# Kernel optimization log

Measured on AMD Instinct MI355X. Metric: run time of the kernel, lower is better.

The kernel has to match this reference:

```python
import jax, jax.numpy as jnp
import numpy as np

WS = (8, 8)          # window size (Wh, Ww)
SS = (4, 4)          # shift size
DIM = 512
HEADS = 16
HD = DIM // HEADS    # 32
D1 = (HD // 2) // 2  # 8
D2 = (HD // 2) - D1  # 8
EPS = 1e-5
B, H, W = 4, 128, 128
HIDDEN = int(DIM * 4.0)  # 2048 (swiglu -> fc1 out = 2*HIDDEN)


def _layer_norm(x, g, b):
    m = jnp.mean(x, -1, keepdims=True)
    v = jnp.mean((x - m) ** 2, -1, keepdims=True)
    return (x - m) * jax.lax.rsqrt(v + EPS) * g + b


def _rope_tables():
    wh, ww = WS
    inv1 = 10000.0 ** (-(jnp.arange(D1, dtype=jnp.float32) / D1))
    inv2 = 10000.0 ** (-(jnp.arange(D2, dtype=jnp.float32) / D2))
    rows = jnp.arange(wh, dtype=jnp.float32)[:, None] * inv1  # (wh, D1)
    cols = jnp.arange(ww, dtype=jnp.float32)[:, None] * inv2  # (ww, D2)
    sin1 = jnp.broadcast_to(jnp.sin(rows)[:, None, :], (wh, ww, D1))
    cos1 = jnp.broadcast_to(jnp.cos(rows)[:, None, :], (wh, ww, D1))
    sin2 = jnp.broadcast_to(jnp.sin(cols)[None, :, :], (wh, ww, D2))
    cos2 = jnp.broadcast_to(jnp.cos(cols)[None, :, :], (wh, ww, D2))
    return sin1, cos1, sin2, cos2


def _rope2d(t, tabs):
    # t: (B_*heads, wh, ww, HD)
    sin1, cos1, sin2, cos2 = tabs
    x11 = t[..., :D1]
    x21 = t[..., D1:D1 + D2]
    x12 = t[..., D1 + D2:D1 + D2 + D1]
    x22 = t[..., D1 + D2 + D1:]
    return jnp.concatenate([
        x11 * cos1 - x12 * sin1,
        x21 * cos2 - x22 * sin2,
        x12 * cos1 + x11 * sin1,
        x22 * cos2 + x21 * sin2,
    ], axis=-1)


def _swin_mask():
    wh, ww = WS
    img = np.zeros((H, W), dtype=np.float32)
    cnt = 0
    for hs in (slice(0, -wh), slice(-wh, -SS[0]), slice(-SS[0], None)):
        for ws in (slice(0, -ww), slice(-ww, -SS[1]), slice(-SS[1], None)):
            img[hs, ws] = cnt
            cnt += 1
    mw = img.reshape(H // wh, wh, W // ww, ww).transpose(0, 2, 1, 3).reshape(-1, wh * ww)
    diff = mw[:, None, :] - mw[:, :, None]
    return jnp.asarray(np.where(diff != 0, -100.0, 0.0).astype(np.float32))


def setup_inputs() -> dict:
    key = jax.random.key(0)
    ks = jax.random.split(key, 14)
    s = 0.02
    return {
        "x": jax.random.normal(ks[0], (B, H, W, DIM), jnp.float32),
        "attn_mask": _swin_mask(),
        "norm1_g": jnp.ones((DIM,), jnp.float32),
        "norm1_b": jnp.zeros((DIM,), jnp.float32),
        "qkv_w": jax.random.normal(ks[1], (3 * DIM, DIM), jnp.float32) * s,
        "qkv_b": jnp.zeros((3 * DIM,), jnp.float32),
        "proj_w": jax.random.normal(ks[2], (DIM, DIM), jnp.float32) * s,
        "proj_b": jnp.zeros((DIM,), jnp.float32),
        "norm2_g": jnp.ones((DIM,), jnp.float32),
        "norm2_b": jnp.zeros((DIM,), jnp.float32),
        "fc1_w": jax.random.normal(ks[3], (2 * HIDDEN, DIM), jnp.float32) * s,
        "fc1_b": jnp.zeros((2 * HIDDEN,), jnp.float32),
        "fc2_w": jax.random.normal(ks[4], (DIM, HIDDEN), jnp.float32) * s,
        "fc2_b": jnp.zeros((DIM,), jnp.float32),
    }


def reference(x, attn_mask, norm1_g, norm1_b, qkv_w, qkv_b, proj_w, proj_b,
              norm2_g, norm2_b, fc1_w, fc1_b, fc2_w, fc2_b):
    wh, ww = WS
    N = wh * ww
    nH, nW = H // wh, W // ww
    nWin = nH * nW
    B_ = B * nWin
    tabs = _rope_tables()

    shortcut = x
    xn = _layer_norm(x, norm1_g, norm1_b)
    # cyclic shift
    xs = jnp.roll(xn, (-SS[0], -SS[1]), axis=(1, 2))
    # window partition: (B,H,W,C) -> (B*nWin, N, C)
    xw = xs.reshape(B, nH, wh, nW, ww, DIM).transpose(0, 1, 3, 2, 4, 5).reshape(B_, N, DIM)

    qkv = xw @ qkv_w.T + qkv_b
    qkv = qkv.reshape(B_, N, 3, HEADS, HD).transpose(2, 0, 3, 1, 4)  # (3,B_,h,N,hd)
    q, k, v = qkv[0], qkv[1], qkv[2]
    # inline 2D RoPE on q,k per window
    q = _rope2d(q.reshape(-1, wh, ww, HD), tabs).reshape(B_, HEADS, N, HD)
    k = _rope2d(k.reshape(-1, wh, ww, HD), tabs).reshape(B_, HEADS, N, HD)

    scale = HD ** -0.5
    attn = jnp.einsum('bhnd,bhmd->bhnm', q * scale, k)
    attn = attn.reshape(B, nWin, HEADS, N, N) + attn_mask[None, :, None]
    attn = jax.nn.softmax(attn.reshape(B_, HEADS, N, N), axis=-1)

    out = jnp.einsum('bhnm,bhmd->bhnd', attn, v).transpose(0, 2, 1, 3).reshape(B_, N, DIM)
    out = out @ proj_w.T + proj_b
    # window reverse + reverse shift
    out = out.reshape(B, nH, nW, wh, ww, DIM).transpose(0, 1, 3, 2, 4, 5).reshape(B, H, W, DIM)
    out = jnp.roll(out, (SS[0], SS[1]), axis=(1, 2))

    x = shortcut + out
    # SwiGLU MLP
    y = _layer_norm(x, norm2_g, norm2_b)
    h = y @ fc1_w.T + fc1_b
    a, gate = jnp.split(h, 2, axis=-1)
    h = jax.nn.silu(gate) * a
    y = h @ fc2_w.T + fc2_b
    return x + y
```

## Files before the change

kernel.cpp:

```cpp
#include <hip/hip_runtime.h>
#include <stdint.h>

typedef __attribute__((ext_vector_type(8))) short bf16x8;
typedef __attribute__((ext_vector_type(4))) float f32x4;
typedef __attribute__((ext_vector_type(4))) int i32x4;
typedef unsigned short u16;

#define GLD_LDS16(g, l) __builtin_amdgcn_global_load_lds( \
    (const __attribute__((address_space(1))) void*)(g),   \
    (__attribute__((address_space(3))) void*)(l), 16, 0, 0)

#define PB() do { __builtin_amdgcn_sched_barrier(0); \
                  __builtin_amdgcn_s_barrier();      \
                  __builtin_amdgcn_sched_barrier(0); } while (0)

#define ACCUM(d, a_, b_) d = __builtin_amdgcn_mfma_f32_16x16x32_bf16(a_, b_, d, 0, 0, 0)
#define ACCI(d, a_, b_)  d = __builtin_amdgcn_mfma_i32_16x16x64_i8(a_, b_, d, 0, 0, 0)

#define INV_A (1.0f / 16384.0f)
#define INV_P (1.0f / 32768.0f)
#define INV_H (1.0f / 65536.0f)

__device__ __forceinline__ u16 f2bf(float f) {
  union { float f; uint32_t u; } a; a.f = f;
  uint32_t u = a.u;
  return (u16)((u + 0x7fffu + ((u >> 16) & 1u)) >> 16);
}
__device__ __forceinline__ float bf2f(u16 h) {
  union { uint32_t u; float f; } a; a.u = ((uint32_t)h) << 16;
  return a.f;
}
__device__ __forceinline__ uint32_t q8x4(float a, float b, float c, float d, float s) {
  int qa = (int)rintf(fminf(fmaxf(a * s, -127.f), 127.f));
  int qb = (int)rintf(fminf(fmaxf(b * s, -127.f), 127.f));
  int qc = (int)rintf(fminf(fmaxf(c * s, -127.f), 127.f));
  int qd = (int)rintf(fminf(fmaxf(d * s, -127.f), 127.f));
  return (qa & 255) | ((qb & 255) << 8) | ((qc & 255) << 16) | ((qd & 255) << 24);
}
__device__ __forceinline__ char q8(float v, float s) {
  return (char)(int)rintf(fminf(fmaxf(v * s, -127.f), 127.f));
}

__global__ __launch_bounds__(256) void ln1_wconv(const float* __restrict__ x,
    const float* __restrict__ gw, const float* __restrict__ bw, char* __restrict__ out,
    const float* __restrict__ qw, const float* __restrict__ pw,
    const float* __restrict__ f1w, const float* __restrict__ f2w,
    char* __restrict__ wb8) {
  int bx = blockIdx.x;
  if (bx >= 16384) {
    int i4 = (bx - 16384) * 1024 + threadIdx.x * 4;
    float w[4];
#pragma unroll
    for (int j = 0; j < 4; j++) {
      int idx = i4 + j;
      if (idx < 786432)        w[j] = qw[idx];
      else if (idx < 1048576)  w[j] = pw[idx - 786432];
      else if (idx < 3145728)  w[j] = f1w[idx - 1048576];
      else                     w[j] = f2w[idx - 3145728];
    }
    *(uint32_t*)(wb8 + i4) = q8x4(w[0], w[1], w[2], w[3], 1024.f);
    return;
  }
  int wid = threadIdx.x >> 6;
  int lane = threadIdx.x & 63;
  int m = (bx << 2) + wid;
  int n = m & 63;
  int bwin = m >> 6;
  int b = bwin >> 8;
  int wi = bwin & 255;
  int h = (((wi >> 4) << 3) + (n >> 3) + 4) & 127;
  int w = (((wi & 15) << 3) + (n & 7) + 4) & 127;
  const float* src = x + (((size_t)((b << 7) + h) << 7) + (size_t)w) * 512;
  int ch = lane << 3;
  float4 v0 = *(const float4*)(src + ch);
  float4 v1 = *(const float4*)(src + ch + 4);
  float vv[8] = {v0.x, v0.y, v0.z, v0.w, v1.x, v1.y, v1.z, v1.w};
  float s = 0.f, s2 = 0.f;
#pragma unroll
  for (int j = 0; j < 8; j++) { s += vv[j]; s2 += vv[j] * vv[j]; }
#pragma unroll
  for (int off = 32; off; off >>= 1) {
    s += __shfl_xor(s, off);
    s2 += __shfl_xor(s2, off);
  }
  float mean = s * (1.f / 512.f);
  float var = s2 * (1.f / 512.f) - mean * mean;
  float rstd = rsqrtf(var + 1e-5f);
  float y[8];
#pragma unroll
  for (int j = 0; j < 8; j++) y[j] = (vv[j] - mean) * rstd * gw[ch + j] + bw[ch + j];
  uint2 o;
  o.x = q8x4(y[0], y[1], y[2], y[3], 16.f);
  o.y = q8x4(y[4], y[5], y[6], y[7], 16.f);
  *(uint2*)(out + ((size_t)m << 9) + ch) = o;
}

__global__ __launch_bounds__(256) void ln2_q8(const u16* __restrict__ sb,
    const float* __restrict__ gw, const float* __restrict__ bw,
    char* __restrict__ out) {
  int wid = threadIdx.x >> 6;
  int lane = threadIdx.x & 63;
  int m = (blockIdx.x << 2) + wid;
  int ch = lane << 3;
  union { uint4 u; u16 hh[8]; } in;
  in.u = *(const uint4*)(sb + ((size_t)m << 9) + ch);
  float vv[8];
#pragma unroll
  for (int j = 0; j < 8; j++) vv[j] = bf2f(in.hh[j]);
  float s = 0.f, s2 = 0.f;
#pragma unroll
  for (int j = 0; j < 8; j++) { s += vv[j]; s2 += vv[j] * vv[j]; }
#pragma unroll
  for (int off = 32; off; off >>= 1) {
    s += __shfl_xor(s, off);
    s2 += __shfl_xor(s2, off);
  }
  float mean = s * (1.f / 512.f);
  float var = s2 * (1.f / 512.f) - mean * mean;
  float rstd = rsqrtf(var + 1e-5f);
  float y[8];
#pragma unroll
  for (int j = 0; j < 8; j++) y[j] = (vv[j] - mean) * rstd * gw[ch + j] + bw[ch + j];
  uint2 o;
  o.x = q8x4(y[0], y[1], y[2], y[3], 16.f);
  o.y = q8x4(y[4], y[5], y[6], y[7], 16.f);
  *(uint2*)(out + ((size_t)m << 9) + ch) = o;
}

template<int EPI, int K>
__global__ __launch_bounds__(512, 1) void gemm8i(
    const char* __restrict__ A, const char* __restrict__ Bw,
    const float* __restrict__ bias, void* __restrict__ outp,
    const float* __restrict__ resid, int NTN) {
  __shared__ __align__(16) char lds[2][4][16384];
  const int NT = K / 128;
  int bid = blockIdx.x;
  int nwg = gridDim.x;
  int wg = (bid & 7) * (nwg >> 3) + (bid >> 3);
  int mt = wg / NTN, nt = wg - mt * NTN;
  int m0 = mt << 8;
  int n0 = (EPI == 3) ? (nt << 7) : (nt << 8);

  int tid = threadIdx.x;
  int wid = tid >> 6, lane = tid & 63;
  int wm = wid >> 2, wn = wid & 3;
  int l15 = lane & 15, lhi = lane >> 4;
  int swz = (lane & 7) << 4;

  int sr0 = tid >> 3;
  int xk = (((tid & 7) ^ ((tid >> 3) & 7)) << 4);

  auto stage = [&](int mat, int hh, int t) {
    if (t >= NT) return;
    char* ld = &lds[t & 1][mat * 2 + hh][0] + (wid << 10);
    const char* g0;
    if (mat == 0) {
      g0 = A + (size_t)(m0 + hh * 128 + sr0) * K + t * 128 + xk;
    } else {
      int rb;
      if (EPI == 3) rb = (hh ? 2048 : 0) + n0 + sr0;
      else          rb = n0 + hh * 128 + sr0;
      g0 = Bw + (size_t)rb * K + t * 128 + xk;
    }
    GLD_LDS16(g0, ld);
    GLD_LDS16(g0 + (size_t)64 * K, ld + 8192);
  };

  i32x4 acc[2][4][2][2] = {};
  i32x4 afr[4][2], b1r[2][2];
  i32x4 b0A[2][2], b0B[2][2];

  int aoffB = (wm * 64 + l15) * 128;
  int boffB = (wn * 32 + l15) * 128;
  int k0b = (lhi * 16) ^ swz;
  int k1b = (64 + lhi * 16) ^ swz;

  stage(0, 0, 0); stage(1, 1, 0); stage(1, 0, 0); stage(0, 1, 0);
  stage(0, 0, 1); stage(1, 1, 1);
  asm volatile("s_waitcnt vmcnt(4)" ::: "memory");
  __builtin_amdgcn_sched_barrier(0);
  __builtin_amdgcn_s_barrier();
  __builtin_amdgcn_sched_barrier(0);
  {
    const char* B00 = &lds[0][2][0];
#pragma unroll
    for (int j = 0; j < 2; j++) {
      b0A[j][0] = *(const i32x4*)&B00[boffB + j * 2048 + k0b];
      b0A[j][1] = *(const i32x4*)&B00[boffB + j * 2048 + k1b];
    }
  }

  auto tile = [&](int s, i32x4 (&b0c)[2][2], i32x4 (&b0n)[2][2]) {
    const char* Ah0 = &lds[s & 1][0][0];
    const char* Ah1 = &lds[s & 1][1][0];
    const char* Bh1 = &lds[s & 1][3][0];
    const char* Bn0 = &lds[(s + 1) & 1][2][0];

#pragma unroll
    for (int i = 0; i < 4; i++) {
      afr[i][0] = *(const i32x4*)&Ah0[aoffB + i * 2048 + k0b];
      afr[i][1] = *(const i32x4*)&Ah0[aoffB + i * 2048 + k1b];
    }
    stage(1, 0, s + 1);
    PB();
    __builtin_amdgcn_s_setprio(1);
#pragma unroll
    for (int i = 0; i < 4; i++)
#pragma unroll
      for (int j = 0; j < 2; j++) {
        ACCI(acc[0][i][0][j], afr[i][0], b0c[j][0]);
        ACCI(acc[0][i][0][j], afr[i][1], b0c[j][1]);
      }
    __builtin_amdgcn_s_setprio(0);
    PB();

#pragma unroll
    for (int j = 0; j < 2; j++) {
      b1r[j][0] = *(const i32x4*)&Bh1[boffB + j * 2048 + k0b];
      b1r[j][1] = *(const i32x4*)&Bh1[boffB + j * 2048 + k1b];
    }
    stage(0, 1, s + 1);
    PB();
    __builtin_amdgcn_s_setprio(1);
#pragma unroll
    for (int i = 0; i < 4; i++)
#pragma unroll
      for (int j = 0; j < 2; j++) {
        ACCI(acc[0][i][1][j], afr[i][0], b1r[j][0]);
        ACCI(acc[0][i][1][j], afr[i][1], b1r[j][1]);
      }
    __builtin_amdgcn_s_setprio(0);
    PB();

#pragma unroll
    for (int i = 0; i < 4; i++) {
      afr[i][0] = *(const i32x4*)&Ah1[aoffB + i * 2048 + k0b];
      afr[i][1] = *(const i32x4*)&Ah1[aoffB + i * 2048 + k1b];
    }
    stage(0, 0, s + 2);
    PB();
    __builtin_amdgcn_s_setprio(1);
#pragma unroll
    for (int i = 0; i < 4; i++)
#pragma unroll
      for (int j = 0; j < 2; j++) {
        ACCI(acc[1][i][1][j], afr[i][0], b1r[j][0]);
        ACCI(acc[1][i][1][j], afr[i][1], b1r[j][1]);
      }
    __builtin_amdgcn_s_setprio(0);
    if (s < NT - 2)       { asm volatile("s_waitcnt vmcnt(4)" ::: "memory"); }
    else if (s == NT - 2) { asm volatile("s_waitcnt vmcnt(2)" ::: "memory"); }
    __builtin_amdgcn_sched_barrier(0);
    __builtin_amdgcn_s_barrier();
    __builtin_amdgcn_sched_barrier(0);

    if (s < NT - 1) {
#pragma unroll
      for (int j = 0; j < 2; j++) {
        b0n[j][0] = *(const i32x4*)&Bn0[boffB + j * 2048 + k0b];
        b0n[j][1] = *(const i32x4*)&Bn0[boffB + j * 2048 + k1b];
      }
    }
    stage(1, 1, s + 2);
    PB();
    __builtin_amdgcn_s_setprio(1);
#pragma unroll
    for (int i = 0; i < 4; i++)
#pragma unroll
      for (int j = 0; j < 2; j++) {
        ACCI(acc[1][i][0][j], afr[i][0], b0c[j][0]);
        ACCI(acc[1][i][0][j], afr[i][1], b0c[j][1]);
      }
    __builtin_amdgcn_s_setprio(0);
    if (s >= NT - 2) { asm volatile("s_waitcnt vmcnt(0)" ::: "memory"); }
    else             { asm volatile("s_waitcnt vmcnt(4)" ::: "memory"); }
    __builtin_amdgcn_sched_barrier(0);
    __builtin_amdgcn_s_barrier();
    __builtin_amdgcn_sched_barrier(0);
  };

  for (int sp = 0; sp < NT; sp += 2) {
    tile(sp, b0A, b0B);
    tile(sp + 1, b0B, b0A);
  }

#pragma unroll
  for (int qm = 0; qm < 2; qm++)
#pragma unroll
    for (int i = 0; i < 4; i++) {
      int row = m0 + qm * 128 + wm * 64 + i * 16 + lhi * 4;
      if (EPI == 0) {
        u16* out = (u16*)outp;
#pragma unroll
        for (int qn = 0; qn < 2; qn++)
#pragma unroll
          for (int j = 0; j < 2; j++) {
            int colb = n0 + qn * 128 + wn * 32 + j * 16;
            int col = colb + l15;
            int sh = colb >> 5;
            int d = (colb & 31) + l15;
            float bv = bias[col];
#pragma unroll
            for (int rg = 0; rg < 4; rg++)
              out[(size_t)sh * 2097152 + (size_t)(row + rg) * 32 + d] =
                  f2bf((float)acc[qm][i][qn][j][rg] * INV_A + bv);
          }
      } else if (EPI == 1) {
        u16* sbw = (u16*)outp;
#pragma unroll
        for (int rg = 0; rg < 4; rg++) {
          int m = row + rg;
          int b = m >> 14, wi2 = (m >> 6) & 255, n = m & 63;
          int h = (((wi2 >> 4) << 3) + (n >> 3) + 4) & 127;
          int w = (((wi2 & 15) << 3) + (n & 7) + 4) & 127;
          size_t pix = (((size_t)((b << 7) + h) << 7) + (size_t)w) << 9;
#pragma unroll
          for (int qn = 0; qn < 2; qn++)
#pragma unroll
            for (int j = 0; j < 2; j++) {
              int col = n0 + qn * 128 + wn * 32 + j * 16 + l15;
              sbw[pix + col] = f2bf(resid[pix + col] +
                                    (float)acc[qm][i][qn][j][rg] * INV_P + bias[col]);
            }
        }
      } else if (EPI == 2) {
        float* out = (float*)outp;
        const u16* sbp = (const u16*)resid;
#pragma unroll
        for (int qn = 0; qn < 2; qn++)
#pragma unroll
          for (int j = 0; j < 2; j++) {
            int col = n0 + qn * 128 + wn * 32 + j * 16 + l15;
            float bv = bias[col];
#pragma unroll
            for (int rg = 0; rg < 4; rg++) {
              size_t idx = (size_t)(row + rg) * 512 + col;
              out[idx] = bf2f(sbp[idx]) + (float)acc[qm][i][qn][j][rg] * INV_H + bv;
            }
          }
      } else {
        char* out = (char*)outp;
#pragma unroll
        for (int j = 0; j < 2; j++) {
          int col = n0 + wn * 32 + j * 16 + l15;
          float ba_ = bias[col], bg_ = bias[col + 2048];
#pragma unroll
          for (int rg = 0; rg < 4; rg++) {
            float av = (float)acc[qm][i][0][j][rg] * INV_A + ba_;
            float gv = (float)acc[qm][i][1][j][rg] * INV_A + bg_;
            float sw = gv / (1.f + __expf(-gv));
            out[(size_t)(row + rg) * 2048 + col] = q8(sw * av, 64.f);
          }
        }
      }
    }
}

__global__ __launch_bounds__(256) void attn_mfma(
    const u16* __restrict__ qkv, char* __restrict__ out) {
  __shared__ __align__(16) char alds[4][15360];
  int tid = threadIdx.x;
  int wid = tid >> 6, lane = tid & 63;
  int bwin = blockIdx.x >> 2;
  int head = ((blockIdx.x & 3) << 2) + wid;
  int wi = bwin & 255;
  int wr = wi >> 4, wc = wi & 15;
  char* Wb = alds[wid];
  u16* Qr = (u16*)Wb;
  u16* Kr = (u16*)(Wb + 5120);
  u16* Vt = (u16*)(Wb + 10240);
  u16* PT = (u16*)Wb;
  int t = lane;
  int l15 = lane & 15, lhi = lane >> 4;
  size_t tok = (size_t)(bwin << 6) + t;
  const u16* qb = qkv + (size_t)head * 2097152 + tok * 32;
  union U { uint4 u; u16 s[8]; };
  U vq[4], vk[4], vv[4];
#pragma unroll
  for (int g = 0; g < 4; g++) {
    vq[g].u = *(const uint4*)(qb + (g << 3));
    vk[g].u = *(const uint4*)(qb + 33554432 + (g << 3));
    vv[g].u = *(const uint4*)(qb + 67108864 + (g << 3));
  }
  float q[32], k[32];
#pragma unroll
  for (int j = 0; j < 32; j++) {
    q[j] = bf2f(vq[j >> 3].s[j & 7]);
    k[j] = bf2f(vk[j >> 3].s[j & 7]);
  }
  int r = t >> 3, c = t & 7;
#pragma unroll
  for (int d = 0; d < 16; d++) {
    float pos = (d < 8) ? (float)r : (float)c;
    int dd = (d < 8) ? d : d - 8;
    float ang = pos * __expf(-(float)dd * 1.1512925465f);
    float sn, cs;
    __sincosf(ang, &sn, &cs);
    float q1 = q[d], q2 = q[d + 16];
    q[d] = q1 * cs - q2 * sn;  q[d + 16] = q2 * cs + q1 * sn;
    float k1 = k[d], k2 = k[d + 16];
    k[d] = k1 * cs - k2 * sn;  k[d + 16] = k2 * cs + k1 * sn;
  }
#pragma unroll
  for (int j = 0; j < 32; j++) q[j] *= 0.17677669529663687f;
#pragma unroll
  for (int sl = 0; sl < 4; sl++) {
    U tq, tk;
#pragma unroll
    for (int j = 0; j < 8; j++) { tq.s[j] = f2bf(q[sl * 8 + j]); tk.s[j] = f2bf(k[sl * 8 + j]); }
    *(uint4*)(Qr + t * 40 + sl * 8) = tq.u;
    *(uint4*)(Kr + t * 40 + sl * 8) = tk.u;
  }
#pragma unroll
  for (int j = 0; j < 32; j++) Vt[j * 72 + t] = vv[j >> 3].s[j & 7];
  bf16x8 kf[4], qf[4];
#pragma unroll
  for (int i = 0; i < 4; i++) {
    kf[i] = *(const bf16x8*)(Kr + (i * 16 + l15) * 40 + lhi * 8);
    qf[i] = *(const bf16x8*)(Qr + (i * 16 + l15) * 40 + lhi * 8);
  }
  f32x4 zz = {0.f, 0.f, 0.f, 0.f};
  f32x4 st[4][4];
#pragma unroll
  for (int mi = 0; mi < 4; mi++)
#pragma unroll
    for (int nj = 0; nj < 4; nj++)
      st[mi][nj] = __builtin_amdgcn_mfma_f32_16x16x32_bf16(kf[mi], qf[nj], zz, 0, 0, 0);
  if (wr == 15 || wc == 15) {
    int idh = (wr == 15) ? ((r >= 4) ? 2 : 1) : 0;
    int idw = (wc == 15) ? ((c >= 4) ? 2 : 1) : 0;
    int code = idh * 3 + idw;
    int cq[4], cm[4][4];
#pragma unroll
    for (int nj = 0; nj < 4; nj++) cq[nj] = __shfl(code, nj * 16 + l15);
#pragma unroll
    for (int mi = 0; mi < 4; mi++)
#pragma unroll
      for (int rg = 0; rg < 4; rg++) cm[mi][rg] = __shfl(code, mi * 16 + lhi * 4 + rg);
#pragma unroll
    for (int mi = 0; mi < 4; mi++)
#pragma unroll
      for (int nj = 0; nj < 4; nj++)
#pragma unroll
        for (int rg = 0; rg < 4; rg++)
          if (cm[mi][rg] != cq[nj]) st[mi][nj][rg] -= 100.f;
  }
  float inv_[4];
#pragma unroll
  for (int nj = 0; nj < 4; nj++) {
    float mx = -1e30f;
#pragma unroll
    for (int mi = 0; mi < 4; mi++)
#pragma unroll
      for (int rg = 0; rg < 4; rg++) mx = fmaxf(mx, st[mi][nj][rg]);
    mx = fmaxf(mx, __shfl_xor(mx, 16));
    mx = fmaxf(mx, __shfl_xor(mx, 32));
    float sum = 0.f;
#pragma unroll
    for (int mi = 0; mi < 4; mi++)
#pragma unroll
      for (int rg = 0; rg < 4; rg++) {
        float p = __expf(st[mi][nj][rg] - mx);
        st[mi][nj][rg] = p;
        sum += p;
      }
    sum += __shfl_xor(sum, 16);
    sum += __shfl_xor(sum, 32);
    inv_[nj] = 1.f / sum;
  }
#pragma unroll
  for (int mi = 0; mi < 4; mi++)
#pragma unroll
    for (int nj = 0; nj < 4; nj++) {
      uint32_t lo, hi;
      asm("v_cvt_pk_bf16_f32 %0, %1, %2" : "=v"(lo) : "v"(st[mi][nj][0]), "v"(st[mi][nj][1]));
      asm("v_cvt_pk_bf16_f32 %0, %1, %2" : "=v"(hi) : "v"(st[mi][nj][2]), "v"(st[mi][nj][3]));
      uint2 pr; pr.x = lo; pr.y = hi;
      *(uint2*)(PT + (nj * 16 + l15) * 72 + mi * 16 + lhi * 4) = pr;
    }
  bf16x8 vf[2][2], pf[4][2];
#pragma unroll
  for (int i = 0; i < 2; i++)
#pragma unroll
    for (int kc = 0; kc < 2; kc++)
      vf[i][kc] = *(const bf16x8*)(Vt + (i * 16 + l15) * 72 + kc * 32 + lhi * 8);
#pragma unroll
  for (int nj = 0; nj < 4; nj++)
#pragma unroll
    for (int kc = 0; kc < 2; kc++)
      pf[nj][kc] = *(const bf16x8*)(PT + (nj * 16 + l15) * 72 + kc * 32 + lhi * 8);
  char* Ot = Wb;
#pragma unroll
  for (int i = 0; i < 2; i++)
#pragma unroll
    for (int nj = 0; nj < 4; nj++) {
      f32x4 o = __builtin_amdgcn_mfma_f32_16x16x32_bf16(vf[i][0], pf[nj][0], zz, 0, 0, 0);
      o = __builtin_amdgcn_mfma_f32_16x16x32_bf16(vf[i][1], pf[nj][1], o, 0, 0, 0);
      float iv32 = inv_[nj] * 32.f;
      uint32_t pk = q8x4(o[0] * iv32, o[1] * iv32, o[2] * iv32, o[3] * iv32, 1.f);
      *(uint32_t*)(Ot + (nj * 16 + l15) * 40 + i * 16 + lhi * 4) = pk;
    }
#pragma unroll
  for (int g = 0; g < 4; g++) {
    int tl = g * 16 + (lane >> 2);
    int ch_ = (lane & 3) << 3;
    uint2 v = *(const uint2*)(Ot + tl * 40 + ch_);
    *(uint2*)(out + (size_t)((bwin << 6) + tl) * 512 + (head << 5) + ch_) = v;
  }
}

extern "C" void kernel_launch(void* const* d_in, const int* in_sizes, int n_in,
                              void* d_out, int out_size, void* d_ws, size_t ws_size,
                              hipStream_t stream) {
  (void)in_sizes; (void)n_in; (void)out_size; (void)ws_size;
  const float* x      = (const float*)d_in[0];
  const float* n1g    = (const float*)d_in[2];
  const float* n1b    = (const float*)d_in[3];
  const float* qkv_w  = (const float*)d_in[4];
  const float* qkv_b  = (const float*)d_in[5];
  const float* proj_w = (const float*)d_in[6];
  const float* proj_b = (const float*)d_in[7];
  const float* n2g    = (const float*)d_in[8];
  const float* n2b    = (const float*)d_in[9];
  const float* fc1_w  = (const float*)d_in[10];
  const float* fc1_b  = (const float*)d_in[11];
  const float* fc2_w  = (const float*)d_in[12];
  const float* fc2_b  = (const float*)d_in[13];

  const size_t MB = 1048576ULL;
  char* ws = (char*)d_ws;
  char* wb8  = ws;
  char* wq8  = wb8;
  char* wp8  = wb8 + 786432;
  char* wf18 = wb8 + 1048576;
  char* wf28 = wb8 + 3145728;
  char* xw8  = ws + 8 * MB;
  char* attn8 = xw8;
  u16*  qkvb = (u16*)(ws + 72 * MB);
  char* hb8  = ws + 8 * MB;
  u16*  sb   = (u16*)(ws + 264 * MB);
  char* yb8  = ws + 328 * MB;

  ln1_wconv<<<20480, 256, 0, stream>>>(x, n1g, n1b, xw8,
                                       qkv_w, proj_w, fc1_w, fc2_w, wb8);
  gemm8i<0, 512><<<1536, 512, 0, stream>>>(xw8, wq8, qkv_b, qkvb, nullptr, 6);
  attn_mfma<<<4096, 256, 0, stream>>>(qkvb, attn8);
  gemm8i<1, 512><<<512, 512, 0, stream>>>(attn8, wp8, proj_b, sb, x, 2);
  ln2_q8<<<16384, 256, 0, stream>>>(sb, n2g, n2b, yb8);
  gemm8i<3, 512><<<4096, 512, 0, stream>>>(yb8, wf18, fc1_b, hb8, nullptr, 16);
  gemm8i<2, 2048><<<512, 512, 0, stream>>>(hb8, wf28, fc2_b, d_out,
                                           (const float*)sb, 2);
}
```

Measured before the change: 572.8 us.

## Shrink int8 GEMM tiles to 128-row, 64-k for higher occupancy

Replaces the 256x256 tile, 128-deep k-step int8 GEMM with a 128-row tile, 64-deep k-step variant that uses about 48KB of LDS instead of 128KB and declares launch bounds allowing several blocks per CU. The pipeline drops to a simple single-stage loop with two LDS buffers and a new XOR swizzle, and grid sizes double. The aim is more resident waves to hide latency, at the cost of less data reuse per tile and more barriers per unit of work.

Measured after the change: 564.7 us, median of 2. About the same (-1.4%).

```diff
diff --git a/kernel.cpp b/kernel.cpp
--- a/kernel.cpp
+++ b/kernel.cpp
@@ -14,7 +14,6 @@
                   __builtin_amdgcn_s_barrier();      \
                   __builtin_amdgcn_sched_barrier(0); } while (0)
 
-#define ACCUM(d, a_, b_) d = __builtin_amdgcn_mfma_f32_16x16x32_bf16(a_, b_, d, 0, 0, 0)
 #define ACCI(d, a_, b_)  d = __builtin_amdgcn_mfma_i32_16x16x64_i8(a_, b_, d, 0, 0, 0)
 
 #define INV_A (1.0f / 16384.0f)
@@ -128,232 +127,165 @@
 }
 
 template<int EPI, int K>
-__global__ __launch_bounds__(512, 1) void gemm8i(
+__global__ __launch_bounds__(512, 4) void gemm2i(
     const char* __restrict__ A, const char* __restrict__ Bw,
     const float* __restrict__ bias, void* __restrict__ outp,
     const float* __restrict__ resid, int NTN) {
-  __shared__ __align__(16) char lds[2][4][16384];
-  const int NT = K / 128;
+  __shared__ __align__(16) char lds[2][3][8192];
+  const int NT = K / 64;
   int bid = blockIdx.x;
   int nwg = gridDim.x;
   int wg = (bid & 7) * (nwg >> 3) + (bid >> 3);
   int mt = wg / NTN, nt = wg - mt * NTN;
-  int m0 = mt << 8;
+  int m0 = mt << 7;
   int n0 = (EPI == 3) ? (nt << 7) : (nt << 8);
 
   int tid = threadIdx.x;
   int wid = tid >> 6, lane = tid & 63;
   int wm = wid >> 2, wn = wid & 3;
   int l15 = lane & 15, lhi = lane >> 4;
-  int swz = (lane & 7) << 4;
-
-  int sr0 = tid >> 3;
-  int xk = (((tid & 7) ^ ((tid >> 3) & 7)) << 4);
-
-  auto stage = [&](int mat, int hh, int t) {
+
+  int sr0 = tid >> 2;
+  int sc = (tid & 3) ^ ((sr0 >> 1) & 3);
+  const char* gA  = A  + (size_t)(m0 + sr0) * K + sc * 16;
+  const char* gB0 = Bw + (size_t)(n0 + sr0) * K + sc * 16;
+  const char* gB1 = (EPI == 3)
+      ? (Bw + (size_t)(2048 + n0 + sr0) * K + sc * 16)
+      : (Bw + (size_t)(n0 + 128 + sr0) * K + sc * 16);
+
+  auto stage = [&](int slot, const char* gp, int t) {
     if (t >= NT) return;
-    char* ld = &lds[t & 1][mat * 2 + hh][0] + (wid << 10);
-    const char* g0;
-    if (mat == 0) {
-      g0 = A + (size_t)(m0 + hh * 128 + sr0) * K + t * 128 + xk;
-    } else {
-      int rb;
-      if (EPI == 3) rb = (hh ? 2048 : 0) + n0 + sr0;
-      else          rb = n0 + hh * 128 + sr0;
-      g0 = Bw + (size_t)rb * K + t * 128 + xk;
-    }
-    GLD_LDS16(g0, ld);
-    GLD_LDS16(g0 + (size_t)64 * K, ld + 8192);
+    char* ld = &lds[t & 1][slot][0] + tid * 16;
+    GLD_LDS16(gp + t * 64, ld);
   };
 
-  i32x4 acc[2][4][2][2] = {};
-  i32x4 afr[4][2], b1r[2][2];
-  i32x4 b0A[2][2], b0B[2][2];
-
-  int aoffB = (wm * 64 + l15) * 128;
-  int boffB = (wn * 32 + l15) * 128;
-  int k0b = (lhi * 16) ^ swz;
-  int k1b = (64 + lhi * 16) ^ swz;
-
-  stage(0, 0, 0); stage(1, 1, 0); stage(1, 0, 0); stage(0, 1, 0);
-  stage(0, 0, 1); stage(1, 1, 1);
-  asm volatile("s_waitcnt vmcnt(4)" ::: "memory");
+  int aoff[4], boff[2];
+#pragma unroll
+  for (int i = 0; i < 4; i++) {
+    int r = wm * 64 + i * 16 + l15;
+    aoff[i] = r * 64 + ((lhi ^ ((r >> 1) & 3)) << 4);
+  }
+#pragma unroll
+  for (int j = 0; j < 2; j++) {
+    int r = wn * 32 + j * 16 + l15;
+    boff[j] = r * 64 + ((lhi ^ ((r >> 1) & 3)) << 4);
+  }
+
+  i32x4 acc[2][4][2] = {};
+  i32x4 afr[4], b0r[2], b1r[2];
+
+  stage(0, gA, 0); stage(1, gB0, 0); stage(2, gB1, 0);
+  stage(0, gA, 1); stage(1, gB0, 1);
+  asm volatile("s_waitcnt vmcnt(2)" ::: "memory");
   __builtin_amdgcn_sched_barrier(0);
   __builtin_amdgcn_s_barrier();
   __builtin_amdgcn_sched_barrier(0);
-  {
-    const char* B00 = &lds[0][2][0];
-#pragma unroll
-    for (int j = 0; j < 2; j++) {
-      b0A[j][0] = *(const i32x4*)&B00[boffB + j * 2048 + k0b];
-      b0A[j][1] = *(const i32x4*)&B00[boffB + j * 2048 + k1b];
-    }
-  }
-
-  auto tile = [&](int s, i32x4 (&b0c)[2][2], i32x4 (&b0n)[2][2]) {
-    const char* Ah0 = &lds[s & 1][0][0];
-    const char* Ah1 = &lds[s & 1][1][0];
-    const char* Bh1 = &lds[s & 1][3][0];
-    const char* Bn0 = &lds[(s + 1) & 1][2][0];
-
-#pragma unroll
-    for (int i = 0; i < 4; i++) {
-      afr[i][0] = *(const i32x4*)&Ah0[aoffB + i * 2048 + k0b];
-      afr[i][1] = *(const i32x4*)&Ah0[aoffB + i * 2048 + k1b];
-    }
-    stage(1, 0, s + 1);
+
+  for (int s = 0; s < NT; ++s) {
+    const char* Ah  = &lds[s & 1][0][0];
+    const char* B0h = &lds[s & 1][1][0];
+    const char* B1h = &lds[s & 1][2][0];
+
+#pragma unroll
+    for (int i = 0; i < 4; i++) afr[i] = *(const i32x4*)&Ah[aoff[i]];
+#pragma unroll
+    for (int j = 0; j < 2; j++) b0r[j] = *(const i32x4*)&B0h[boff[j]];
+    stage(2, gB1, s + 1);
     PB();
     __builtin_amdgcn_s_setprio(1);
 #pragma unroll
     for (int i = 0; i < 4; i++)
 #pragma unroll
-      for (int j = 0; j < 2; j++) {
-        ACCI(acc[0][i][0][j], afr[i][0], b0c[j][0]);
-        ACCI(acc[0][i][0][j], afr[i][1], b0c[j][1]);
-      }
+      for (int j = 0; j < 2; j++) ACCI(acc[0][i][j], afr[i], b0r[j]);
     __builtin_amdgcn_s_setprio(0);
     PB();
 
 #pragma unroll
-    for (int j = 0; j < 2; j++) {
-      b1r[j][0] = *(const i32x4*)&Bh1[boffB + j * 2048 + k0b];
-      b1r[j][1] = *(const i32x4*)&Bh1[boffB + j * 2048 + k1b];
-    }
-    stage(0, 1, s + 1);
+    for (int j = 0; j < 2; j++) b1r[j] = *(const i32x4*)&B1h[boff[j]];
+    stage(0, gA, s + 2);
+    stage(1, gB0, s + 2);
     PB();
     __builtin_amdgcn_s_setprio(1);
 #pragma unroll
     for (int i = 0; i < 4; i++)
 #pragma unroll
-      for (int j = 0; j < 2; j++) {
-        ACCI(acc[0][i][1][j], afr[i][0], b1r[j][0]);
-        ACCI(acc[0][i][1][j], afr[i][1], b1r[j][1]);
-      }
+      for (int j = 0; j < 2; j++) ACCI(acc[1][i][j], afr[i], b1r[j]);
     __builtin_amdgcn_s_setprio(0);
-    PB();
-
-#pragma unroll
-    for (int i = 0; i < 4; i++) {
-      afr[i][0] = *(const i32x4*)&Ah1[aoffB + i * 2048 + k0b];
-      afr[i][1] = *(const i32x4*)&Ah1[aoffB + i * 2048 + k1b];
-    }
-    stage(0, 0, s + 2);
-    PB();
-    __builtin_amdgcn_s_setprio(1);
-#pragma unroll
-    for (int i = 0; i < 4; i++)
-#pragma unroll
-      for (int j = 0; j < 2; j++) {
-        ACCI(acc[1][i][1][j], afr[i][0], b1r[j][0]);
-        ACCI(acc[1][i][1][j], afr[i][1], b1r[j][1]);
-      }
-    __builtin_amdgcn_s_setprio(0);
-    if (s < NT - 2)       { asm volatile("s_waitcnt vmcnt(4)" ::: "memory"); }
-    else if (s == NT - 2) { asm volatile("s_waitcnt vmcnt(2)" ::: "memory"); }
+    if (s >= NT - 2) { asm volatile("s_waitcnt vmcnt(0)" ::: "memory"); }
+    else             { asm volatile("s_waitcnt vmcnt(2)" ::: "memory"); }
     __builtin_amdgcn_sched_barrier(0);
     __builtin_amdgcn_s_barrier();
     __builtin_amdgcn_sched_barrier(0);
-
-    if (s < NT - 1) {
+  }
+
+#pragma unroll
+  for (int i = 0; i < 4; i++) {
+    int row = m0 + wm * 64 + i * 16 + lhi * 4;
+    if (EPI == 0) {
+      u16* out = (u16*)outp;
+#pragma unroll
+      for (int h = 0; h < 2; h++)
+#pragma unroll
+        for (int j = 0; j < 2; j++) {
+          int colb = n0 + h * 128 + wn * 32 + j * 16;
+          int col = colb + l15;
+          int sh = colb >> 5;
+          int d = (colb & 31) + l15;
+          float bv = bias[col];
+#pragma unroll
+          for (int rg = 0; rg < 4; rg++)
+            out[(size_t)sh * 2097152 + (size_t)(row + rg) * 32 + d] =
+                f2bf((float)acc[h][i][j][rg] * INV_A + bv);
+        }
+    } else if (EPI == 1) {
+      u16* sbw = (u16*)outp;
+#pragma unroll
+      for (int rg = 0; rg < 4; rg++) {
+        int m = row + rg;
+        int b = m >> 14, wi2 = (m >> 6) & 255, n = m & 63;
+        int hh = (((wi2 >> 4) << 3) + (n >> 3) + 4) & 127;
+        int w = (((wi2 & 15) << 3) + (n & 7) + 4) & 127;
+        size_t pix = (((size_t)((b << 7) + hh) << 7) + (size_t)w) << 9;
+#pragma unroll
+        for (int h = 0; h < 2; h++)
+#pragma unroll
+          for (int j = 0; j < 2; j++) {
+            int col = n0 + h * 128 + wn * 32 + j * 16 + l15;
+            sbw[pix + col] = f2bf(resid[pix + col] +
+                                  (float)acc[h][i][j][rg] * INV_P + bias[col]);
+          }
+      }
+    } else if (EPI == 2) {
+      float* out = (float*)outp;
+      const u16* sbp = (const u16*)resid;
+#pragma unroll
+      for (int h = 0; h < 2; h++)
+#pragma unroll
+        for (int j = 0; j < 2; j++) {
+          int col = n0 + h * 128 + wn * 32 + j * 16 + l15;
+          float bv = bias[col];
+#pragma unroll
+          for (int rg = 0; rg < 4; rg++) {
+            size_t idx = (size_t)(row + rg) * 512 + col;
+            out[idx] = bf2f(sbp[idx]) + (float)acc[h][i][j][rg] * INV_H + bv;
+          }
+        }
+    } else {
+      char* out = (char*)outp;
 #pragma unroll
       for (int j = 0; j < 2; j++) {
-        b0n[j][0] = *(const i32x4*)&Bn0[boffB + j * 2048 + k0b];
-        b0n[j][1] = *(const i32x4*)&Bn0[boffB + j * 2048 + k1b];
-      }
-    }
-    stage(1, 1, s + 2);
-    PB();
-    __builtin_amdgcn_s_setprio(1);
-#pragma unroll
-    for (int i = 0; i < 4; i++)
-#pragma unroll
-      for (int j = 0; j < 2; j++) {
-        ACCI(acc[1][i][0][j], afr[i][0], b0c[j][0]);
-        ACCI(acc[1][i][0][j], afr[i][1], b0c[j][1]);
-      }
-    __builtin_amdgcn_s_setprio(0);
-    if (s >= NT - 2) { asm volatile("s_waitcnt vmcnt(0)" ::: "memory"); }
-    else             { asm volatile("s_waitcnt vmcnt(4)" ::: "memory"); }
-    __builtin_amdgcn_sched_barrier(0);
-    __builtin_amdgcn_s_barrier();
-    __builtin_amdgcn_sched_barrier(0);
-  };
-
-  for (int sp = 0; sp < NT; sp += 2) {
-    tile(sp, b0A, b0B);
-    tile(sp + 1, b0B, b0A);
-  }
-
-#pragma unroll
-  for (int qm = 0; qm < 2; qm++)
-#pragma unroll
-    for (int i = 0; i < 4; i++) {
-      int row = m0 + qm * 128 + wm * 64 + i * 16 + lhi * 4;
-      if (EPI == 0) {
-        u16* out = (u16*)outp;
-#pragma unroll
-        for (int qn = 0; qn < 2; qn++)
-#pragma unroll
-          for (int j = 0; j < 2; j++) {
-            int colb = n0 + qn * 128 + wn * 32 + j * 16;
-            int col = colb + l15;
-            int sh = colb >> 5;
-            int d = (colb & 31) + l15;
-            float bv = bias[col];
-#pragma unroll
-            for (int rg = 0; rg < 4; rg++)
-              out[(size_t)sh * 2097152 + (size_t)(row + rg) * 32 + d] =
-                  f2bf((float)acc[qm][i][qn][j][rg] * INV_A + bv);
-          }
-      } else if (EPI == 1) {
-        u16* sbw = (u16*)outp;
+        int col = n0 + wn * 32 + j * 16 + l15;
+        float ba_ = bias[col], bg_ = bias[col + 2048];
 #pragma unroll
         for (int rg = 0; rg < 4; rg++) {
-          int m = row + rg;
-          int b = m >> 14, wi2 = (m >> 6) & 255, n = m & 63;
-          int h = (((wi2 >> 4) << 3) + (n >> 3) + 4) & 127;
-          int w = (((wi2 & 15) << 3) + (n & 7) + 4) & 127;
-          size_t pix = (((size_t)((b << 7) + h) << 7) + (size_t)w) << 9;
-#pragma unroll
-          for (int qn = 0; qn < 2; qn++)
-#pragma unroll
-            for (int j = 0; j < 2; j++) {
-              int col = n0 + qn * 128 + wn * 32 + j * 16 + l15;
-              sbw[pix + col] = f2bf(resid[pix + col] +
-                                    (float)acc[qm][i][qn][j][rg] * INV_P + bias[col]);
-            }
-        }
-      } else if (EPI == 2) {
-        float* out = (float*)outp;
-        const u16* sbp = (const u16*)resid;
-#pragma unroll
-        for (int qn = 0; qn < 2; qn++)
-#pragma unroll
-          for (int j = 0; j < 2; j++) {
-            int col = n0 + qn * 128 + wn * 32 + j * 16 + l15;
-            float bv = bias[col];
-#pragma unroll
-            for (int rg = 0; rg < 4; rg++) {
-              size_t idx = (size_t)(row + rg) * 512 + col;
-              out[idx] = bf2f(sbp[idx]) + (float)acc[qm][i][qn][j][rg] * INV_H + bv;
-            }
-          }
-      } else {
-        char* out = (char*)outp;
-#pragma unroll
-        for (int j = 0; j < 2; j++) {
-          int col = n0 + wn * 32 + j * 16 + l15;
-          float ba_ = bias[col], bg_ = bias[col + 2048];
-#pragma unroll
-          for (int rg = 0; rg < 4; rg++) {
-            float av = (float)acc[qm][i][0][j][rg] * INV_A + ba_;
-            float gv = (float)acc[qm][i][1][j][rg] * INV_A + bg_;
-            float sw = gv / (1.f + __expf(-gv));
-            out[(size_t)(row + rg) * 2048 + col] = q8(sw * av, 64.f);
-          }
+          float av = (float)acc[0][i][j][rg] * INV_A + ba_;
+          float gv = (float)acc[1][i][j][rg] * INV_A + bg_;
+          float sw = gv / (1.f + __expf(-gv));
+          out[(size_t)(row + rg) * 2048 + col] = q8(sw * av, 64.f);
         }
       }
     }
+  }
 }
 
 __global__ __launch_bounds__(256) void attn_mfma(
@@ -543,11 +475,11 @@
 
   ln1_wconv<<<20480, 256, 0, stream>>>(x, n1g, n1b, xw8,
                                        qkv_w, proj_w, fc1_w, fc2_w, wb8);
-  gemm8i<0, 512><<<1536, 512, 0, stream>>>(xw8, wq8, qkv_b, qkvb, nullptr, 6);
+  gemm2i<0, 512><<<3072, 512, 0, stream>>>(xw8, wq8, qkv_b, qkvb, nullptr, 6);
   attn_mfma<<<4096, 256, 0, stream>>>(qkvb, attn8);
-  gemm8i<1, 512><<<512, 512, 0, stream>>>(attn8, wp8, proj_b, sb, x, 2);
+  gemm2i<1, 512><<<1024, 512, 0, stream>>>(attn8, wp8, proj_b, sb, x, 2);
   ln2_q8<<<16384, 256, 0, stream>>>(sb, n2g, n2b, yb8);
-  gemm8i<3, 512><<<4096, 512, 0, stream>>>(yb8, wf18, fc1_b, hb8, nullptr, 16);
-  gemm8i<2, 2048><<<512, 512, 0, stream>>>(hb8, wf28, fc2_b, d_out,
-                                           (const float*)sb, 2);
-}
+  gemm2i<3, 512><<<8192, 512, 0, stream>>>(yb8, wf18, fc1_b, hb8, nullptr, 16);
+  gemm2i<2, 2048><<<1024, 512, 0, stream>>>(hb8, wf28, fc2_b, d_out,
+                                            (const float*)sb, 2);
+}
```
